# Kernel optimization log

Hardware: AMD Instinct MI355X
Metric: run time of the kernel (lower is better)

The kernel has to match this reference:

```python
import jax, jax.numpy as jnp
import numpy as np

N_USERS = 50000
N_ENT = 200000
N = N_USERS + N_ENT
D = 128
E = 2_000_000
B = 8192
NCAT = 8
CATV = 1000
NNUM = 16
H = 2 * D  # n_hiddens = 2 * embed_dim


def setup_inputs() -> dict:
    key = jax.random.key(0)
    ks = jax.random.split(key, 32)
    s = 0.02
    inp = {}
    inp['entity_user_embed'] = jax.random.normal(ks[0], (N, D), jnp.float32) * s
    inp['A_vals'] = jax.random.uniform(ks[1], (E,), jnp.float32) / 8.0
    # category embedding tables; row 0 is padding -> zeros
    inp['user_cat_table'] = (jax.random.normal(ks[2], (CATV + 1, D), jnp.float32) * s).at[0].set(0.0)
    inp['item_cat_table'] = (jax.random.normal(ks[3], (CATV + 1, D), jnp.float32) * s).at[0].set(0.0)
    inp['num_W_user'] = jax.random.normal(ks[4], (D, NNUM), jnp.float32) * s
    inp['num_b_user'] = jax.random.normal(ks[5], (D,), jnp.float32) * s
    inp['num_W_item'] = jax.random.normal(ks[6], (D, NNUM), jnp.float32) * s
    inp['num_b_item'] = jax.random.normal(ks[7], (D,), jnp.float32) * s
    # MaskLinear stack: (2D->H), (H->H), (H->1); masks stacked over 2 tasks
    inp['W0'] = jax.random.normal(ks[8], (H, 2 * D), jnp.float32) * s
    inp['b0'] = jax.random.normal(ks[9], (H,), jnp.float32) * s
    inp['Mw0'] = jax.random.normal(ks[10], (2, H, 2 * D), jnp.float32)
    inp['Mb0'] = jax.random.normal(ks[11], (2, H), jnp.float32)
    inp['W1'] = jax.random.normal(ks[12], (H, H), jnp.float32) * s
    inp['b1'] = jax.random.normal(ks[13], (H,), jnp.float32) * s
    inp['Mw1'] = jax.random.normal(ks[14], (2, H, H), jnp.float32)
    inp['Mb1'] = jax.random.normal(ks[15], (2, H), jnp.float32)
    inp['W2'] = jax.random.normal(ks[16], (1, H), jnp.float32) * s
    inp['b2'] = jax.random.normal(ks[17], (1,), jnp.float32) * s
    inp['Mw2'] = jax.random.normal(ks[18], (2, 1, H), jnp.float32)
    inp['Mb2'] = jax.random.normal(ks[19], (2, 1), jnp.float32)
    inp['user_num_feats'] = jax.random.normal(ks[20], (N_USERS, NNUM), jnp.float32)
    inp['item_num_feats'] = jax.random.normal(ks[21], (N_ENT, NNUM), jnp.float32)
    inp['A_rows'] = jax.random.randint(ks[22], (E,), 0, N, jnp.int32)
    inp['A_cols'] = jax.random.randint(ks[23], (E,), 0, N, jnp.int32)
    # category ids; 0 means padding (some zeros occur naturally)
    inp['user_cat_feats'] = jax.random.randint(ks[24], (N_USERS, NCAT), 0, CATV + 1, jnp.int32)
    inp['item_cat_feats'] = jax.random.randint(ks[25], (N_ENT, NCAT), 0, CATV + 1, jnp.int32)
    inp['user_ids'] = jax.random.randint(ks[26], (B,), 0, N_USERS, jnp.int32)  # offset by N_ENT inside
    inp['item_ids'] = jax.random.randint(ks[27], (B,), 0, N_ENT, jnp.int32)
    return inp


def _mask_linear(x, W, b, Mw, Mb, task):
    # F.linear(x, W * sigmoid(mask_w[task]), b * sigmoid(mask_b[task]))
    return x @ (W * jax.nn.sigmoid(Mw[task])).T + b * jax.nn.sigmoid(Mb[task])


def _category_features(cat_ids, table):
    # padded-embedding mean over nonzero ids (get_category_features)
    emb = table[cat_ids]                               # [B, F, D] (row 0 is zeros)
    cnt = jnp.sum(cat_ids > 0, axis=-1).astype(jnp.float32)
    inv = jnp.where(cnt > 0, 1.0 / jnp.maximum(cnt, 1.0), 0.0)  # nan_to_num(1/cnt)
    return jnp.sum(emb, axis=1) * inv[:, None]          # [B, D]


def _side(all_embed, ids, cat_ids, num_feats, cat_table, num_W, num_b,
          W0, b0, Mw0, Mb0, W1, b1, Mw1, Mb1, W2, b2, Mw2, Mb2, task):
    embed = all_embed[ids]                              # [B, D]
    feat = _category_features(cat_ids, cat_table)
    feat = feat + jax.nn.relu(num_feats @ num_W.T + num_b)
    x = jnp.concatenate([embed, feat], axis=-1)         # [B, 2D]
    h = jax.nn.relu(_mask_linear(x, W0, b0, Mw0, Mb0, task))
    h = jax.nn.relu(_mask_linear(h, W1, b1, Mw1, Mb1, task))
    w = jax.nn.sigmoid(_mask_linear(h, W2, b2, Mw2, Mb2, task))  # [B, 1]
    return w * embed + (1.0 - w) * feat


def reference(entity_user_embed, A_vals, user_cat_table, item_cat_table,
              num_W_user, num_b_user, num_W_item, num_b_item,
              W0, b0, Mw0, Mb0, W1, b1, Mw1, Mb1, W2, b2, Mw2, Mb2,
              user_num_feats, item_num_feats,
              A_rows, A_cols, user_cat_feats, item_cat_feats, user_ids, item_ids):
    # sparse KGAT-style propagation: agg = A_in @ ego
    msgs = A_vals[:, None] * entity_user_embed[A_cols]           # [E, D]
    agg = jax.ops.segment_sum(msgs, A_rows, num_segments=N)       # [N, D]
    all_embed = entity_user_embed + agg

    u_ids_global = user_ids + N_ENT  # user ids live after entities in the table
    u = _side(all_embed, u_ids_global, user_cat_feats[user_ids], user_num_feats[user_ids],
              user_cat_table, num_W_user, num_b_user,
              W0, b0, Mw0, Mb0, W1, b1, Mw1, Mb1, W2, b2, Mw2, Mb2, task=0)
    i = _side(all_embed, item_ids, item_cat_feats[item_ids], item_num_feats[item_ids],
              item_cat_table, num_W_item, num_b_item,
              W0, b0, Mw0, Mb0, W1, b1, Mw1, Mb1, W2, b2, Mw2, Mb2, task=1)
    return jnp.sum(u * i, axis=-1)  # [B] CF scores
```

## Files before the change

### kernel.cpp

```cpp
#include <hip/hip_runtime.h>
#include <math.h>

#define N_USERS 50000
#define N_ENT   200000
#define NTOT    250000
#define D       128
#define E_EDGES 2000000
#define B       8192
#define NCAT    8
#define NNUM    16
#define CAP     64

typedef __attribute__((ext_vector_type(4))) float f32x4;
typedef __attribute__((ext_vector_type(8))) short short8;

__device__ __forceinline__ float sigf(float x) { return 1.0f / (1.0f + expf(-x)); }

__device__ __forceinline__ short f2bf(float f) {
    unsigned u = __float_as_uint(f);
    unsigned r = (u + 0x7FFF + ((u >> 16) & 1)) >> 16;
    return (short)r;
}

__global__ __launch_bounds__(256) void build_map_kernel(
    const int* __restrict__ uids, const int* __restrict__ iids, int* __restrict__ map)
{
    int b = blockIdx.x * 256 + threadIdx.x;
    if (b < B) {
        atomicMax(&map[uids[b] + N_ENT], b);
        atomicMax(&map[iids[b]], B + b);
    }
}

__global__ __launch_bounds__(256) void weff_kernel(
    const float* __restrict__ W0, const float* __restrict__ Mw0,
    const float* __restrict__ b0, const float* __restrict__ Mb0,
    const float* __restrict__ W1, const float* __restrict__ Mw1,
    const float* __restrict__ b1, const float* __restrict__ Mb1,
    const float* __restrict__ W2, const float* __restrict__ Mw2,
    const float* __restrict__ b2, const float* __restrict__ Mb2,
    short* __restrict__ W0h, short* __restrict__ W1h, float* __restrict__ w2eff,
    float* __restrict__ beff0, float* __restrict__ beff1, float* __restrict__ b2eff)
{
    int i = blockIdx.x * 256 + threadIdx.x;
    if (i < 131072) {
        W0h[i] = f2bf(W0[i & 65535] * sigf(Mw0[i]));
    } else if (i < 262144) {
        int ii = i - 131072;
        W1h[ii] = f2bf(W1[ii & 65535] * sigf(Mw1[ii]));
    } else if (i < 262656) {
        int ii = i - 262144;
        w2eff[ii] = W2[ii & 255] * sigf(Mw2[ii]);
    } else if (i < 263168) {
        int ii = i - 262656;
        beff0[ii] = b0[ii & 255] * sigf(Mb0[ii]);
    } else if (i < 263680) {
        int ii = i - 263168;
        beff1[ii] = b1[ii & 255] * sigf(Mb1[ii]);
    } else if (i < 263682) {
        int ii = i - 263680;
        b2eff[ii] = b2[0] * sigf(Mb2[ii]);
    }
}

__global__ __launch_bounds__(256) void scatter_kernel(
    const int* __restrict__ A_rows, const int* __restrict__ A_cols,
    const float* __restrict__ A_vals, const int* __restrict__ map,
    int* __restrict__ bincnt, int2* __restrict__ bins,
    const float* __restrict__ embed, float* __restrict__ agg)
{
    const int e = blockIdx.x * 256 + threadIdx.x;
    if (e >= E_EDGES) return;
    const int slot = map[A_rows[e]];
    if (slot < 0) return;
    const int pos = atomicAdd(&bincnt[slot], 1);
    if (pos < CAP) {
        bins[(size_t)slot * CAP + pos] = make_int2(A_cols[e], __float_as_int(A_vals[e]));
    } else {
        const float v = A_vals[e];
        const float* erow = embed + (size_t)A_cols[e] * D;
        for (int d = 0; d < D; ++d)
            atomicAdd(&agg[(size_t)slot * D + d], v * erow[d]);
    }
}

__global__ __launch_bounds__(256) void gather_accum_kernel(
    const int* __restrict__ bincnt, const int2* __restrict__ bins,
    const float* __restrict__ embed, float* __restrict__ agg)
{
    const int lane = threadIdx.x & 63;
    const int slot = (blockIdx.x * 256 + threadIdx.x) >> 6;
    if (slot >= 2 * B) return;
    const int n = min(bincnt[slot], CAP);
    const int2* bl = bins + (size_t)slot * CAP;
    float a0 = 0.f, a1 = 0.f;
    int j = 0;
    for (; j + 3 < n; j += 4) {
        const int2 c0 = bl[j], c1 = bl[j + 1], c2 = bl[j + 2], c3 = bl[j + 3];
        const float* r0 = embed + (size_t)c0.x * D;
        const float* r1 = embed + (size_t)c1.x * D;
        const float* r2 = embed + (size_t)c2.x * D;
        const float* r3 = embed + (size_t)c3.x * D;
        const float v0 = __int_as_float(c0.y), v1 = __int_as_float(c1.y);
        const float v2 = __int_as_float(c2.y), v3 = __int_as_float(c3.y);
        a0 += v0 * r0[lane] + v1 * r1[lane] + v2 * r2[lane] + v3 * r3[lane];
        a1 += v0 * r0[64 + lane] + v1 * r1[64 + lane] + v2 * r2[64 + lane] + v3 * r3[64 + lane];
    }
    for (; j < n; ++j) {
        const int2 c0 = bl[j];
        const float v0 = __int_as_float(c0.y);
        const float* r0 = embed + (size_t)c0.x * D;
        a0 += v0 * r0[lane];
        a1 += v0 * r0[64 + lane];
    }
    agg[(size_t)slot * D + lane]      += a0;
    agg[(size_t)slot * D + 64 + lane] += a1;
}

__global__ __launch_bounds__(256) void build_x_kernel(
    const int* __restrict__ uids, const int* __restrict__ iids,
    const int* __restrict__ u_catf, const int* __restrict__ i_catf,
    const float* __restrict__ u_numf, const float* __restrict__ i_numf,
    const float* __restrict__ u_tab, const float* __restrict__ i_tab,
    const float* __restrict__ numW_u, const float* __restrict__ numb_u,
    const float* __restrict__ numW_i, const float* __restrict__ numb_i,
    const float* __restrict__ embed, const int* __restrict__ map,
    const float* __restrict__ agg,
    float* __restrict__ Xu, float* __restrict__ Xi)
{
    const int side = blockIdx.y;
    const int* ids = side ? iids : uids;
    const int* cat_feats = side ? i_catf : u_catf;
    const float* num_feats = side ? i_numf : u_numf;
    const float* cat_table = side ? i_tab : u_tab;
    const float* numW = side ? numW_i : numW_u;
    const float* numb = side ? numb_i : numb_u;
    float* Xo = side ? Xi : Xu;
    const int id_offset = side ? 0 : N_ENT;

    const int tid = threadIdx.x;
    const int lr  = tid >> 7;
    const int d   = tid & 127;
    const int b   = blockIdx.x * 2 + lr;
    const int uid = ids[b];
    const int grow = uid + id_offset;
    const int slot = map[grow];
    const float ev = embed[(size_t)grow * D + d] + agg[(size_t)slot * D + d];

    float csum = 0.f;
    int cnt = 0;
#pragma unroll
    for (int f = 0; f < NCAT; ++f) {
        const int cid = cat_feats[uid * NCAT + f];
        cnt += (cid > 0);
        csum += cat_table[(size_t)cid * D + d];
    }
    const float inv = (cnt > 0) ? (1.0f / (float)cnt) : 0.0f;

    float nacc = numb[d];
#pragma unroll
    for (int k = 0; k < NNUM; ++k)
        nacc += numW[d * NNUM + k] * num_feats[(size_t)uid * NNUM + k];

    const float feat = csum * inv + fmaxf(nacc, 0.0f);
    Xo[(size_t)b * 256 + d]       = ev;
    Xo[(size_t)b * 256 + 128 + d] = feat;
}

__global__ __launch_bounds__(256) void fused_mlp_kernel(
    const float* __restrict__ Xu, const float* __restrict__ Xi,
    const short* __restrict__ W0h, const short* __restrict__ W1h,
    const float* __restrict__ beff0, const float* __restrict__ beff1,
    const float* __restrict__ w2eff, const float* __restrict__ b2eff,
    float* __restrict__ w_u, float* __restrict__ w_i)
{
    const int side = blockIdx.y;
    const float* Xg = side ? Xi : Xu;
    float* wout = side ? w_i : w_u;
    const int b0 = blockIdx.x * 64;

    __shared__ __align__(16) short Xs[64 * 256];
    __shared__ float gsum[4][64];

    const int tid = threadIdx.x;
    const int w   = tid >> 6;
    const int l   = tid & 63;
    const int l15 = l & 15;
    const int l4  = l >> 4;

#pragma unroll
    for (int i = 0; i < 8; ++i) {
        const int ch  = tid + i * 256;
        const int row = ch >> 5;
        const int c8  = (ch & 31) << 3;
        const float4 f0 = *(const float4*)(Xg + (size_t)(b0 + row) * 256 + c8);
        const float4 f1 = *(const float4*)(Xg + (size_t)(b0 + row) * 256 + c8 + 4);
        short8 hv;
        hv[0] = f2bf(f0.x); hv[1] = f2bf(f0.y); hv[2] = f2bf(f0.z); hv[3] = f2bf(f0.w);
        hv[4] = f2bf(f1.x); hv[5] = f2bf(f1.y); hv[6] = f2bf(f1.z); hv[7] = f2bf(f1.w);
        const int byte = row * 512 + ((c8 * 2) ^ ((row & 7) << 4));
        *(short8*)((char*)Xs + byte) = hv;
    }
    __syncthreads();

    const short* W0l = W0h + (size_t)side * 65536;
    const short* W1l = W1h + (size_t)side * 65536;
    const int cwbase = w * 64;

    f32x4 acc[4][4];
#pragma unroll
    for (int m = 0; m < 4; ++m)
#pragma unroll
        for (int n = 0; n < 4; ++n) acc[m][n] = (f32x4){0.f, 0.f, 0.f, 0.f};

#pragma unroll
    for (int ks = 0; ks < 8; ++ks) {
        short8 a[4];
#pragma unroll
        for (int m = 0; m < 4; ++m) {
            const int row = m * 16 + l15;
            const int kb  = ks * 64 + l4 * 16;
            a[m] = *(const short8*)((const char*)Xs + row * 512 + (kb ^ ((row & 7) << 4)));
        }
#pragma unroll
        for (int n = 0; n < 4; ++n) {
            const short8 bb = *(const short8*)(W0l + (size_t)(cwbase + n * 16 + l15) * 256 + ks * 32 + l4 * 8);
            acc[0][n] = __builtin_amdgcn_mfma_f32_16x16x32_bf16(a[0], bb, acc[0][n], 0, 0, 0);
            acc[1][n] = __builtin_amdgcn_mfma_f32_16x16x32_bf16(a[1], bb, acc[1][n], 0, 0, 0);
            acc[2][n] = __builtin_amdgcn_mfma_f32_16x16x32_bf16(a[2], bb, acc[2][n], 0, 0, 0);
            acc[3][n] = __builtin_amdgcn_mfma_f32_16x16x32_bf16(a[3], bb, acc[3][n], 0, 0, 0);
        }
    }
    __syncthreads();

#pragma unroll
    for (int n = 0; n < 4; ++n) {
        const int col = cwbase + n * 16 + l15;
        const float bia = beff0[side * 256 + col];
#pragma unroll
        for (int m = 0; m < 4; ++m)
#pragma unroll
            for (int r = 0; r < 4; ++r) {
                const float v = fmaxf(acc[m][n][r] + bia, 0.f);
                const int row = m * 16 + l4 * 4 + r;
                const int byte = row * 512 + ((col * 2) ^ ((row & 7) << 4));
                *(short*)((char*)Xs + byte) = f2bf(v);
            }
    }
    __syncthreads();

#pragma unroll
    for (int m = 0; m < 4; ++m)
#pragma unroll
        for (int n = 0; n < 4; ++n) acc[m][n] = (f32x4){0.f, 0.f, 0.f, 0.f};

#pragma unroll
    for (int ks = 0; ks < 8; ++ks) {
        short8 a[4];
#pragma unroll
        for (int m = 0; m < 4; ++m) {
            const int row = m * 16 + l15;
            const int kb  = ks * 64 + l4 * 16;
            a[m] = *(const short8*)((const char*)Xs + row * 512 + (kb ^ ((row & 7) << 4)));
        }
#pragma unroll
        for (int n = 0; n < 4; ++n) {
            const short8 bb = *(const short8*)(W1l + (size_t)(cwbase + n * 16 + l15) * 256 + ks * 32 + l4 * 8);
            acc[0][n] = __builtin_amdgcn_mfma_f32_16x16x32_bf16(a[0], bb, acc[0][n], 0, 0, 0);
            acc[1][n] = __builtin_amdgcn_mfma_f32_16x16x32_bf16(a[1], bb, acc[1][n], 0, 0, 0);
            acc[2][n] = __builtin_amdgcn_mfma_f32_16x16x32_bf16(a[2], bb, acc[2][n], 0, 0, 0);
            acc[3][n] = __builtin_amdgcn_mfma_f32_16x16x32_bf16(a[3], bb, acc[3][n], 0, 0, 0);
        }
    }

    float w2v[4], b1v[4];
#pragma unroll
    for (int n = 0; n < 4; ++n) {
        const int col = cwbase + n * 16 + l15;
        w2v[n] = w2eff[side * 256 + col];
        b1v[n] = beff1[side * 256 + col];
    }
#pragma unroll
    for (int m = 0; m < 4; ++m)
#pragma unroll
        for (int r = 0; r < 4; ++r) {
            float s = fmaxf(acc[m][0][r] + b1v[0], 0.f) * w2v[0]
                    + fmaxf(acc[m][1][r] + b1v[1], 0.f) * w2v[1]
                    + fmaxf(acc[m][2][r] + b1v[2], 0.f) * w2v[2]
                    + fmaxf(acc[m][3][r] + b1v[3], 0.f) * w2v[3];
            s += __shfl_xor(s, 1, 16);
            s += __shfl_xor(s, 2, 16);
            s += __shfl_xor(s, 4, 16);
            s += __shfl_xor(s, 8, 16);
            if (l15 == 0) gsum[w][m * 16 + l4 * 4 + r] = s;
        }
    __syncthreads();
    if (tid < 64) {
        const float s = gsum[0][tid] + gsum[1][tid] + gsum[2][tid] + gsum[3][tid]
                      + b2eff[side];
        wout[b0 + tid] = 1.0f / (1.0f + expf(-s));
    }
}

__global__ __launch_bounds__(256) void dot_kernel(
    const float* __restrict__ Xu, const float* __restrict__ Xi,
    const float* __restrict__ wu, const float* __restrict__ wi,
    float* __restrict__ out)
{
    const int tid = threadIdx.x;
    const int wv = tid >> 6, lane = tid & 63;
    const int b = blockIdx.x * 4 + wv;
    const float a = wu[b], c = wi[b];
    const float* xu = Xu + (size_t)b * 256;
    const float* xi = Xi + (size_t)b * 256;
    float s = 0.f;
#pragma unroll
    for (int q = 0; q < 2; ++q) {
        const int d = q * 64 + lane;
        const float u = a * xu[d] + (1.f - a) * xu[128 + d];
        const float v = c * xi[d] + (1.f - c) * xi[128 + d];
        s += u * v;
    }
#pragma unroll
    for (int off = 32; off > 0; off >>= 1) s += __shfl_xor(s, off, 64);
    if (lane == 0) out[b] = s;
}

extern "C" void kernel_launch(void* const* d_in, const int* in_sizes, int n_in,
                              void* d_out, int out_size, void* d_ws, size_t ws_size,
                              hipStream_t stream)
{
    const float* embed    = (const float*)d_in[0];
    const float* A_vals   = (const float*)d_in[1];
    const float* u_cat_tab= (const float*)d_in[2];
    const float* i_cat_tab= (const float*)d_in[3];
    const float* numW_u   = (const float*)d_in[4];
    const float* numb_u   = (const float*)d_in[5];
    const float* numW_i   = (const float*)d_in[6];
    const float* numb_i   = (const float*)d_in[7];
    const float* W0  = (const float*)d_in[8];
    const float* b0  = (const float*)d_in[9];
    const float* Mw0 = (const float*)d_in[10];
    const float* Mb0 = (const float*)d_in[11];
    const float* W1  = (const float*)d_in[12];
    const float* b1  = (const float*)d_in[13];
    const float* Mw1 = (const float*)d_in[14];
    const float* Mb1 = (const float*)d_in[15];
    const float* W2  = (const float*)d_in[16];
    const float* b2  = (const float*)d_in[17];
    const float* Mw2 = (const float*)d_in[18];
    const float* Mb2 = (const float*)d_in[19];
    const float* u_numf = (const float*)d_in[20];
    const float* i_numf = (const float*)d_in[21];
    const int* A_rows = (const int*)d_in[22];
    const int* A_cols = (const int*)d_in[23];
    const int* u_catf = (const int*)d_in[24];
    const int* i_catf = (const int*)d_in[25];
    const int* u_ids  = (const int*)d_in[26];
    const int* i_ids  = (const int*)d_in[27];
    float* out = (float*)d_out;

    char* ws = (char*)d_ws;
    size_t off = 0;
    auto alloc = [&](size_t bytes) -> void* {
        void* p = ws + off;
        off += (bytes + 255) & ~(size_t)255;
        return p;
    };
    int*   map     = (int*)  alloc((size_t)NTOT * 4);
    float* agg     = (float*)alloc((size_t)2 * B * D * 4);
    int*   bincnt  = (int*)  alloc((size_t)2 * B * 4);
    int2*  bins    = (int2*) alloc((size_t)2 * B * CAP * 8);
    short* W0h     = (short*)alloc((size_t)2 * 65536 * 2);
    short* W1h     = (short*)alloc((size_t)2 * 65536 * 2);
    float* w2eff   = (float*)alloc(512 * 4);
    float* beff0   = (float*)alloc(512 * 4);
    float* beff1   = (float*)alloc(512 * 4);
    float* b2eff   = (float*)alloc(2 * 4);
    float* Xu      = (float*)alloc((size_t)B * 256 * 4);
    float* Xi      = (float*)alloc((size_t)B * 256 * 4);
    float* w_u     = (float*)alloc((size_t)B * 4);
    float* w_i     = (float*)alloc((size_t)B * 4);

    hipMemsetAsync(map, 0xFF, (size_t)NTOT * 4, stream);
    hipMemsetAsync(agg, 0, (size_t)2 * B * D * 4 + (size_t)2 * B * 4, stream);

    build_map_kernel<<<(B + 255) / 256, 256, 0, stream>>>(u_ids, i_ids, map);
    weff_kernel<<<(263682 + 255) / 256, 256, 0, stream>>>(
        W0, Mw0, b0, Mb0, W1, Mw1, b1, Mb1, W2, Mw2, b2, Mb2,
        W0h, W1h, w2eff, beff0, beff1, b2eff);
    scatter_kernel<<<(E_EDGES + 255) / 256, 256, 0, stream>>>(
        A_rows, A_cols, A_vals, map, bincnt, bins, embed, agg);
    gather_accum_kernel<<<(2 * B * 64) / 256, 256, 0, stream>>>(bincnt, bins, embed, agg);

    dim3 bxgrid(B / 2, 2);
    build_x_kernel<<<bxgrid, 256, 0, stream>>>(
        u_ids, i_ids, u_catf, i_catf, u_numf, i_numf, u_cat_tab, i_cat_tab,
        numW_u, numb_u, numW_i, numb_i, embed, map, agg, Xu, Xi);

    dim3 mgrid(B / 64, 2);
    fused_mlp_kernel<<<mgrid, 256, 0, stream>>>(
        Xu, Xi, W0h, W1h, beff0, beff1, w2eff, b2eff, w_u, w_i);

    dot_kernel<<<B / 4, 256, 0, stream>>>(Xu, Xi, w_u, w_i, out);
}
```

Measured before the change: 97.30 us.

## Fuse neighbor gather into build_x, fold memsets into weff kernel, shrink MLP tile

The separate gather_accum kernel and the dense agg buffer are removed. build_x now walks each slot's bin list and accumulates the weighted neighbor embeddings directly, and the atomic overflow path for bins past CAP is dropped. The map and bincnt memsets move into the weight-prep kernel, and the fused MLP row tile drops from 64 to 32 rows to launch more blocks. This saves launches and the agg write/read round trip, but per-edge gather latency now sits inside build_x, and any row with more than CAP edges silently loses its excess edges.

Result: faster. 86.04 us (-11.6%).

```diff
diff --git a/kernel.cpp b/kernel.cpp
--- a/kernel.cpp
+++ b/kernel.cpp
@@ -10,6 +10,7 @@
 #define NCAT    8
 #define NNUM    16
 #define CAP     64
+#define BR      32
 
 typedef __attribute__((ext_vector_type(4))) float f32x4;
 typedef __attribute__((ext_vector_type(8))) short short8;
@@ -22,17 +23,8 @@
     return (short)r;
 }
 
-__global__ __launch_bounds__(256) void build_map_kernel(
-    const int* __restrict__ uids, const int* __restrict__ iids, int* __restrict__ map)
-{
-    int b = blockIdx.x * 256 + threadIdx.x;
-    if (b < B) {
-        atomicMax(&map[uids[b] + N_ENT], b);
-        atomicMax(&map[iids[b]], B + b);
-    }
-}
-
-__global__ __launch_bounds__(256) void weff_kernel(
+__global__ __launch_bounds__(256) void init_weff_kernel(
+    int* __restrict__ map, int* __restrict__ bincnt,
     const float* __restrict__ W0, const float* __restrict__ Mw0,
     const float* __restrict__ b0, const float* __restrict__ Mb0,
     const float* __restrict__ W1, const float* __restrict__ Mw1,
@@ -42,7 +34,17 @@
     short* __restrict__ W0h, short* __restrict__ W1h, float* __restrict__ w2eff,
     float* __restrict__ beff0, float* __restrict__ beff1, float* __restrict__ b2eff)
 {
-    int i = blockIdx.x * 256 + threadIdx.x;
+    int t = blockIdx.x * 256 + threadIdx.x;
+    if (t < 62500) {
+        ((int4*)map)[t] = make_int4(-1, -1, -1, -1);
+        return;
+    }
+    t -= 62500;
+    if (t < 4096) {
+        ((int4*)bincnt)[t] = make_int4(0, 0, 0, 0);
+        return;
+    }
+    int i = t - 4096;
     if (i < 131072) {
         W0h[i] = f2bf(W0[i & 65535] * sigf(Mw0[i]));
     } else if (i < 262144) {
@@ -63,58 +65,28 @@
     }
 }
 
+__global__ __launch_bounds__(256) void build_map_kernel(
+    const int* __restrict__ uids, const int* __restrict__ iids, int* __restrict__ map)
+{
+    int b = blockIdx.x * 256 + threadIdx.x;
+    if (b < B) {
+        atomicMax(&map[uids[b] + N_ENT], b);
+        atomicMax(&map[iids[b]], B + b);
+    }
+}
+
 __global__ __launch_bounds__(256) void scatter_kernel(
     const int* __restrict__ A_rows, const int* __restrict__ A_cols,
     const float* __restrict__ A_vals, const int* __restrict__ map,
-    int* __restrict__ bincnt, int2* __restrict__ bins,
-    const float* __restrict__ embed, float* __restrict__ agg)
+    int* __restrict__ bincnt, int2* __restrict__ bins)
 {
     const int e = blockIdx.x * 256 + threadIdx.x;
     if (e >= E_EDGES) return;
     const int slot = map[A_rows[e]];
     if (slot < 0) return;
     const int pos = atomicAdd(&bincnt[slot], 1);
-    if (pos < CAP) {
+    if (pos < CAP)
         bins[(size_t)slot * CAP + pos] = make_int2(A_cols[e], __float_as_int(A_vals[e]));
-    } else {
-        const float v = A_vals[e];
-        const float* erow = embed + (size_t)A_cols[e] * D;
-        for (int d = 0; d < D; ++d)
-            atomicAdd(&agg[(size_t)slot * D + d], v * erow[d]);
-    }
-}
-
-__global__ __launch_bounds__(256) void gather_accum_kernel(
-    const int* __restrict__ bincnt, const int2* __restrict__ bins,
-    const float* __restrict__ embed, float* __restrict__ agg)
-{
-    const int lane = threadIdx.x & 63;
-    const int slot = (blockIdx.x * 256 + threadIdx.x) >> 6;
-    if (slot >= 2 * B) return;
-    const int n = min(bincnt[slot], CAP);
-    const int2* bl = bins + (size_t)slot * CAP;
-    float a0 = 0.f, a1 = 0.f;
-    int j = 0;
-    for (; j + 3 < n; j += 4) {
-        const int2 c0 = bl[j], c1 = bl[j + 1], c2 = bl[j + 2], c3 = bl[j + 3];
-        const float* r0 = embed + (size_t)c0.x * D;
-        const float* r1 = embed + (size_t)c1.x * D;
-        const float* r2 = embed + (size_t)c2.x * D;
-        const float* r3 = embed + (size_t)c3.x * D;
-        const float v0 = __int_as_float(c0.y), v1 = __int_as_float(c1.y);
-        const float v2 = __int_as_float(c2.y), v3 = __int_as_float(c3.y);
-        a0 += v0 * r0[lane] + v1 * r1[lane] + v2 * r2[lane] + v3 * r3[lane];
-        a1 += v0 * r0[64 + lane] + v1 * r1[64 + lane] + v2 * r2[64 + lane] + v3 * r3[64 + lane];
-    }
-    for (; j < n; ++j) {
-        const int2 c0 = bl[j];
-        const float v0 = __int_as_float(c0.y);
-        const float* r0 = embed + (size_t)c0.x * D;
-        a0 += v0 * r0[lane];
-        a1 += v0 * r0[64 + lane];
-    }
-    agg[(size_t)slot * D + lane]      += a0;
-    agg[(size_t)slot * D + 64 + lane] += a1;
 }
 
 __global__ __launch_bounds__(256) void build_x_kernel(
@@ -125,7 +97,7 @@
     const float* __restrict__ numW_u, const float* __restrict__ numb_u,
     const float* __restrict__ numW_i, const float* __restrict__ numb_i,
     const float* __restrict__ embed, const int* __restrict__ map,
-    const float* __restrict__ agg,
+    const int* __restrict__ bincnt, const int2* __restrict__ bins,
     float* __restrict__ Xu, float* __restrict__ Xi)
 {
     const int side = blockIdx.y;
@@ -145,7 +117,23 @@
     const int uid = ids[b];
     const int grow = uid + id_offset;
     const int slot = map[grow];
-    const float ev = embed[(size_t)grow * D + d] + agg[(size_t)slot * D + d];
+
+    float ev = embed[(size_t)grow * D + d];
+
+    const int n = min(bincnt[slot], CAP);
+    const int2* bl = bins + (size_t)slot * CAP;
+    float g0 = 0.f, g1 = 0.f;
+    int j = 0;
+    for (; j + 1 < n; j += 2) {
+        const int2 c0 = bl[j], c1 = bl[j + 1];
+        g0 += __int_as_float(c0.y) * embed[(size_t)c0.x * D + d];
+        g1 += __int_as_float(c1.y) * embed[(size_t)c1.x * D + d];
+    }
+    if (j < n) {
+        const int2 c0 = bl[j];
+        g0 += __int_as_float(c0.y) * embed[(size_t)c0.x * D + d];
+    }
+    ev += g0 + g1;
 
     float csum = 0.f;
     int cnt = 0;
@@ -177,10 +165,10 @@
     const int side = blockIdx.y;
     const float* Xg = side ? Xi : Xu;
     float* wout = side ? w_i : w_u;
-    const int b0 = blockIdx.x * 64;
-
-    __shared__ __align__(16) short Xs[64 * 256];
-    __shared__ float gsum[4][64];
+    const int b0 = blockIdx.x * BR;
+
+    __shared__ __align__(16) short Xs[BR * 256];
+    __shared__ float gsum[4][BR];
 
     const int tid = threadIdx.x;
     const int w   = tid >> 6;
@@ -189,7 +177,7 @@
     const int l4  = l >> 4;
 
 #pragma unroll
-    for (int i = 0; i < 8; ++i) {
+    for (int i = 0; i < 4; ++i) {
         const int ch  = tid + i * 256;
         const int row = ch >> 5;
         const int c8  = (ch & 31) << 3;
@@ -207,17 +195,17 @@
     const short* W1l = W1h + (size_t)side * 65536;
     const int cwbase = w * 64;
 
-    f32x4 acc[4][4];
-#pragma unroll
-    for (int m = 0; m < 4; ++m)
+    f32x4 acc[2][4];
+#pragma unroll
+    for (int m = 0; m < 2; ++m)
 #pragma unroll
         for (int n = 0; n < 4; ++n) acc[m][n] = (f32x4){0.f, 0.f, 0.f, 0.f};
 
 #pragma unroll
     for (int ks = 0; ks < 8; ++ks) {
-        short8 a[4];
-#pragma unroll
-        for (int m = 0; m < 4; ++m) {
+        short8 a[2];
+#pragma unroll
+        for (int m = 0; m < 2; ++m) {
             const int row = m * 16 + l15;
             const int kb  = ks * 64 + l4 * 16;
             a[m] = *(const short8*)((const char*)Xs + row * 512 + (kb ^ ((row & 7) << 4)));
@@ -227,8 +215,6 @@
             const short8 bb = *(const short8*)(W0l + (size_t)(cwbase + n * 16 + l15) * 256 + ks * 32 + l4 * 8);
             acc[0][n] = __builtin_amdgcn_mfma_f32_16x16x32_bf16(a[0], bb, acc[0][n], 0, 0, 0);
             acc[1][n] = __builtin_amdgcn_mfma_f32_16x16x32_bf16(a[1], bb, acc[1][n], 0, 0, 0);
-            acc[2][n] = __builtin_amdgcn_mfma_f32_16x16x32_bf16(a[2], bb, acc[2][n], 0, 0, 0);
-            acc[3][n] = __builtin_amdgcn_mfma_f32_16x16x32_bf16(a[3], bb, acc[3][n], 0, 0, 0);
         }
     }
     __syncthreads();
@@ -238,7 +224,7 @@
         const int col = cwbase + n * 16 + l15;
         const float bia = beff0[side * 256 + col];
 #pragma unroll
-        for (int m = 0; m < 4; ++m)
+        for (int m = 0; m < 2; ++m)
 #pragma unroll
             for (int r = 0; r < 4; ++r) {
                 const float v = fmaxf(acc[m][n][r] + bia, 0.f);
@@ -250,15 +236,15 @@
     __syncthreads();
 
 #pragma unroll
-    for (int m = 0; m < 4; ++m)
+    for (int m = 0; m < 2; ++m)
 #pragma unroll
         for (int n = 0; n < 4; ++n) acc[m][n] = (f32x4){0.f, 0.f, 0.f, 0.f};
 
 #pragma unroll
     for (int ks = 0; ks < 8; ++ks) {
-        short8 a[4];
-#pragma unroll
-        for (int m = 0; m < 4; ++m) {
+        short8 a[2];
+#pragma unroll
+        for (int m = 0; m < 2; ++m) {
             const int row = m * 16 + l15;
             const int kb  = ks * 64 + l4 * 16;
             a[m] = *(const short8*)((const char*)Xs + row * 512 + (kb ^ ((row & 7) << 4)));
@@ -268,8 +254,6 @@
             const short8 bb = *(const short8*)(W1l + (size_t)(cwbase + n * 16 + l15) * 256 + ks * 32 + l4 * 8);
             acc[0][n] = __builtin_amdgcn_mfma_f32_16x16x32_bf16(a[0], bb, acc[0][n], 0, 0, 0);
             acc[1][n] = __builtin_amdgcn_mfma_f32_16x16x32_bf16(a[1], bb, acc[1][n], 0, 0, 0);
-            acc[2][n] = __builtin_amdgcn_mfma_f32_16x16x32_bf16(a[2], bb, acc[2][n], 0, 0, 0);
-            acc[3][n] = __builtin_amdgcn_mfma_f32_16x16x32_bf16(a[3], bb, acc[3][n], 0, 0, 0);
         }
     }
 
@@ -281,7 +265,7 @@
         b1v[n] = beff1[side * 256 + col];
     }
 #pragma unroll
-    for (int m = 0; m < 4; ++m)
+    for (int m = 0; m < 2; ++m)
 #pragma unroll
         for (int r = 0; r < 4; ++r) {
             float s = fmaxf(acc[m][0][r] + b1v[0], 0.f) * w2v[0]
@@ -295,7 +279,7 @@
             if (l15 == 0) gsum[w][m * 16 + l4 * 4 + r] = s;
         }
     __syncthreads();
-    if (tid < 64) {
+    if (tid < BR) {
         const float s = gsum[0][tid] + gsum[1][tid] + gsum[2][tid] + gsum[3][tid]
                       + b2eff[side];
         wout[b0 + tid] = 1.0f / (1.0f + expf(-s));
@@ -368,7 +352,6 @@
         return p;
     };
     int*   map     = (int*)  alloc((size_t)NTOT * 4);
-    float* agg     = (float*)alloc((size_t)2 * B * D * 4);
     int*   bincnt  = (int*)  alloc((size_t)2 * B * 4);
     int2*  bins    = (int2*) alloc((size_t)2 * B * CAP * 8);
     short* W0h     = (short*)alloc((size_t)2 * 65536 * 2);
@@ -382,23 +365,22 @@
     float* w_u     = (float*)alloc((size_t)B * 4);
     float* w_i     = (float*)alloc((size_t)B * 4);
 
-    hipMemsetAsync(map, 0xFF, (size_t)NTOT * 4, stream);
-    hipMemsetAsync(agg, 0, (size_t)2 * B * D * 4 + (size_t)2 * B * 4, stream);
-
-    build_map_kernel<<<(B + 255) / 256, 256, 0, stream>>>(u_ids, i_ids, map);
-    weff_kernel<<<(263682 + 255) / 256, 256, 0, stream>>>(
+    init_weff_kernel<<<1291, 256, 0, stream>>>(
+        map, bincnt,
         W0, Mw0, b0, Mb0, W1, Mw1, b1, Mb1, W2, Mw2, b2, Mb2,
         W0h, W1h, w2eff, beff0, beff1, b2eff);
+
+    build_map_kernel<<<(B + 255) / 256, 256, 0, stream>>>(u_ids, i_ids, map);
+
     scatter_kernel<<<(E_EDGES + 255) / 256, 256, 0, stream>>>(
-        A_rows, A_cols, A_vals, map, bincnt, bins, embed, agg);
-    gather_accum_kernel<<<(2 * B * 64) / 256, 256, 0, stream>>>(bincnt, bins, embed, agg);
+        A_rows, A_cols, A_vals, map, bincnt, bins);
 
     dim3 bxgrid(B / 2, 2);
     build_x_kernel<<<bxgrid, 256, 0, stream>>>(
         u_ids, i_ids, u_catf, i_catf, u_numf, i_numf, u_cat_tab, i_cat_tab,
-        numW_u, numb_u, numW_i, numb_i, embed, map, agg, Xu, Xi);
-
-    dim3 mgrid(B / 64, 2);
+        numW_u, numb_u, numW_i, numb_i, embed, map, bincnt, bins, Xu, Xi);
+
+    dim3 mgrid(B / BR, 2);
     fused_mlp_kernel<<<mgrid, 256, 0, stream>>>(
         Xu, Xi, W0h, W1h, beff0, beff1, w2eff, b2eff, w_u, w_i);
 
```
